# Kernel tuning notes

Measured on AMD Instinct MI355X. Metric: run time of the kernel, lower is better.

The kernel has to match this reference:

```python
import jax, jax.numpy as jnp
import numpy as np

SEQ_LEN, BATCH, INPUT, HID, LAYERS, TARGET_LEN = 120, 2048, 6, 64, 4, 120


def _cell(x_t, h, c, Wih, Whh, b):
    # torch LSTM gate order: input, forget, cell(g), output
    gates = x_t @ Wih.T + h @ Whh.T + b  # [B, 4H]
    i, f, g, o = jnp.split(gates, 4, axis=-1)
    c_new = jax.nn.sigmoid(f) * c + jax.nn.sigmoid(i) * jnp.tanh(g)
    h_new = jax.nn.sigmoid(o) * jnp.tanh(c_new)
    return h_new, c_new


def _stack_step(h, c, x_t, Wih0, Wih, Whh, b):
    # one time step through all stacked layers; h, c: [L, B, H]
    hs, cs = [], []
    inp = x_t
    L = Whh.shape[0]
    for l in range(L):
        W = Wih0 if l == 0 else Wih[l - 1]
        hn, cn = _cell(inp, h[l], c[l], W, Whh[l], b[l])
        hs.append(hn)
        cs.append(cn)
        inp = hn
    return jnp.stack(hs), jnp.stack(cs), inp


def setup_inputs() -> dict:
    key = jax.random.key(0)
    ks = jax.random.split(key, 11)
    s = 1.0 / np.sqrt(HID)  # torch LSTM uniform init scale
    u = lambda k, shp: jax.random.uniform(k, shp, jnp.float32, -s, s)
    return {
        "x": jax.random.normal(ks[0], (SEQ_LEN, BATCH, INPUT), jnp.float32),
        "enc_Wih0": u(ks[1], (4 * HID, INPUT)),
        "enc_Wih": u(ks[2], (LAYERS - 1, 4 * HID, HID)),
        "enc_Whh": u(ks[3], (LAYERS, 4 * HID, HID)),
        "enc_b": u(ks[4], (LAYERS, 4 * HID)),
        "dec_Wih0": u(ks[5], (4 * HID, INPUT)),
        "dec_Wih": u(ks[6], (LAYERS - 1, 4 * HID, HID)),
        "dec_Whh": u(ks[7], (LAYERS, 4 * HID, HID)),
        "dec_b": u(ks[8], (LAYERS, 4 * HID)),
        "lin_W": u(ks[9], (INPUT, HID)),
        "lin_b": u(ks[10], (INPUT,)),
        "target_len": TARGET_LEN,
    }


def reference(x, enc_Wih0, enc_Wih, enc_Whh, enc_b,
              dec_Wih0, dec_Wih, dec_Whh, dec_b, lin_W, lin_b, target_len):
    L, B, H = enc_Whh.shape[0], x.shape[1], enc_Whh.shape[-1]
    h0 = jnp.zeros((L, B, H), x.dtype)

    # ---- encoder: stacked LSTM over the input sequence (zero init state) ----
    def enc_step(carry, x_t):
        h, c = carry
        h, c, _ = _stack_step(h, c, x_t, enc_Wih0, enc_Wih, enc_Whh, enc_b)
        return (h, c), None

    (h, c), _ = jax.lax.scan(enc_step, (h0, h0), x)

    # ---- decoder: recursive one-step decode for target_len steps ----
    def dec_step(carry, _):
        h, c, inp = carry
        h, c, top = _stack_step(h, c, inp, dec_Wih0, dec_Wih, dec_Whh, dec_b)
        out = top @ lin_W.T + lin_b  # [B, INPUT]
        return (h, c, out), out

    last_in = x[-1]  # decoder seeded with last observed frame
    _, outputs = jax.lax.scan(dec_step, (h, c, last_in), None, length=target_len)
    return outputs  # [target_len, B, INPUT]
```

## Files before the change

### kernel.cpp

```cpp
#include <hip/hip_runtime.h>


#define S_LEN 120
#define BATCH 2048
#define NIN   6
#define H     64
#define NL    4
#define TLEN  120

#define HPAD 72

#define FRAGS_HALF 60
#define PACK_H8    (2 * FRAGS_HALF * 4 * 64)
#define PROJ_H8    (2 * 64)
#define NPACK      ((PACK_H8 + PROJ_H8) * 8)
#define EPACK_EL   (256 * 64 * 8)
#define NTOT       (NPACK + EPACK_EL)

#define PERM(kk) ((((kk) & 3) << 4) | ((kk) >> 2))
#define PI(c)    ((((c) & 15) << 2) | ((c) >> 4))

typedef _Float16 h8    __attribute__((ext_vector_type(8)));
typedef _Float16 h4    __attribute__((ext_vector_type(4)));
typedef float    f32x4 __attribute__((ext_vector_type(4)));

__global__ void prep_weights(const float* __restrict__ eWih0,
                             const float* __restrict__ eWih,
                             const float* __restrict__ eWhh,
                             const float* __restrict__ dWih0,
                             const float* __restrict__ dWih,
                             const float* __restrict__ dWhh,
                             const float* __restrict__ linW,
                             _Float16* __restrict__ wq) {
  int idx = blockIdx.x * blockDim.x + threadIdx.x;
  if (idx >= NTOT) return;

  if (idx >= NPACK) {
    int p    = idx - NPACK;
    int j    = p & 7;
    int lane = (p >> 3) & 63;
    int fe   = p >> 9;
    int kt   = fe & 3, nt = (fe >> 2) & 15, l = fe >> 6;
    int g    = nt * 16 + (lane & 15);
    int koff = ((lane >> 4) << 3) + j;
    float v = 0.0f;
    if (l == 0) {
      if (kt == 0)      v = (koff < NIN) ? eWih0[g * NIN + koff] : 0.0f;
      else if (kt == 1) v = 0.0f;
      else { int kk = (kt - 2) * 32 + koff; v = eWhh[g * H + PERM(kk)]; }
    } else {
      if (kt < 2) { int kk = kt * 32 + koff;
                    v = eWih[((l - 1) * 256 + g) * H + PERM(kk)]; }
      else        { int kk = (kt - 2) * 32 + koff;
                    v = eWhh[(l * 256 + g) * H + PERM(kk)]; }
    }
    wq[idx] = (_Float16)v;
    return;
  }

  if (idx >= PACK_H8 * 8) {
    int p    = idx - PACK_H8 * 8;
    int j    = p & 7;
    int lane = (p >> 3) & 63;
    int fr   = p >> 9;
    int m    = lane & 15;
    int k    = fr * 32 + ((lane >> 4) << 3) + j;
    wq[idx] = (_Float16)((m < NIN) ? linW[m * H + k] : 0.0f);
    return;
  }

  const int j    = idx & 7;
  const int lane = (idx >> 3) & 63;
  const int wv   = (idx >> 9) & 3;
  const int fh   = idx >> 11;
  const int f    = fh % FRAGS_HALF;
  const int half = fh / FRAGS_HALF;
  const float* Wi0 = half ? dWih0 : eWih0;
  const float* Wi  = half ? dWih  : eWih;
  const float* Wh  = half ? dWhh  : eWhh;
  int l, q, kt;
  if (f < 12) { l = 0; q = f / 3; kt = f % 3; }
  else        { int ff = f - 12; l = 1 + ff / 16; ff %= 16; q = ff / 4; kt = ff % 4; }
  const int g    = q * 64 + wv * 16 + (lane & 15);
  const int k_in = ((lane >> 4) << 3) + j;
  float v;
  if (l == 0) {
    if (kt == 0) v = (k_in < NIN) ? Wi0[g * NIN + k_in] : 0.0f;
    else         v = Wh[g * H + (kt - 1) * 32 + k_in];
  } else {
    if (kt < 2) v = Wi[((l - 1) * 256 + g) * H + kt * 32 + k_in];
    else        v = Wh[(l * 256 + g) * H + (kt - 2) * 32 + k_in];
  }
  wq[idx] = (_Float16)v;
}

__device__ __forceinline__ float rcpf(float x) { return __builtin_amdgcn_rcpf(x); }
__device__ __forceinline__ float sigf(float x) { return rcpf(1.0f + __expf(-x)); }
__device__ __forceinline__ float tanhf_(float x) {
  float e = __expf(2.0f * x);
  return 1.0f - 2.0f * rcpf(e + 1.0f);
}
__device__ __forceinline__ f32x4 mf(h8 a, h8 b, f32x4 c) {
  return __builtin_amdgcn_mfma_f32_16x16x32_f16(a, b, c, 0, 0, 0);
}
#define SPLAT(v) ((f32x4){(v), (v), (v), (v)})

__device__ __forceinline__ void cell_ew(f32x4 g0, f32x4 g1, f32x4 g2, f32x4 g3,
                                        f32x4& c, _Float16* outbuf,
                                        int quad, int r16, int wv) {
  #pragma unroll
  for (int r = 0; r < 4; r++) {
    float gi = sigf(g0[r]);
    float gf = sigf(g1[r]);
    float gg = tanhf_(g2[r]);
    float go = sigf(g3[r]);
    c[r] = fmaf(gf, c[r], gi * gg);
    outbuf[(quad * 4 + r) * HPAD + wv * 16 + r16] = (_Float16)(go * tanhf_(c[r]));
  }
}
__device__ __forceinline__ void fireH(const h8 (&w)[16], h8 ai0, h8 ai1,
                                      const f32x4 (&ac)[4], f32x4& c,
                                      _Float16* outbuf, int quad, int r16, int wv) {
  f32x4 g0 = mf(ai1, w[1],  mf(ai0, w[0],  ac[0]));
  f32x4 g1 = mf(ai1, w[5],  mf(ai0, w[4],  ac[1]));
  f32x4 g2 = mf(ai1, w[9],  mf(ai0, w[8],  ac[2]));
  f32x4 g3 = mf(ai1, w[13], mf(ai0, w[12], ac[3]));
  cell_ew(g0, g1, g2, g3, c, outbuf, quad, r16, wv);
}
__device__ __forceinline__ void precH(const h8 (&w)[16], h8 ar0, h8 ar1,
                                      f32x4 b, f32x4 (&ac)[4]) {
  ac[0] = mf(ar1, w[3],  mf(ar0, w[2],  SPLAT(b[0])));
  ac[1] = mf(ar1, w[7],  mf(ar0, w[6],  SPLAT(b[1])));
  ac[2] = mf(ar1, w[11], mf(ar0, w[10], SPLAT(b[2])));
  ac[3] = mf(ar1, w[15], mf(ar0, w[14], SPLAT(b[3])));
}
__device__ __forceinline__ void fire0(const h8 (&w)[12], h8 ax,
                                      const f32x4 (&ac)[4], f32x4& c,
                                      _Float16* outbuf, int quad, int r16, int wv) {
  f32x4 g0 = mf(ax, w[0], ac[0]);
  f32x4 g1 = mf(ax, w[3], ac[1]);
  f32x4 g2 = mf(ax, w[6], ac[2]);
  f32x4 g3 = mf(ax, w[9], ac[3]);
  cell_ew(g0, g1, g2, g3, c, outbuf, quad, r16, wv);
}
__device__ __forceinline__ void prec0(const h8 (&w)[12], h8 ar0, h8 ar1,
                                      f32x4 b, f32x4 (&ac)[4]) {
  ac[0] = mf(ar1, w[2],  mf(ar0, w[1],  SPLAT(b[0])));
  ac[1] = mf(ar1, w[5],  mf(ar0, w[4],  SPLAT(b[1])));
  ac[2] = mf(ar1, w[8],  mf(ar0, w[7],  SPLAT(b[2])));
  ac[3] = mf(ar1, w[11], mf(ar0, w[10], SPLAT(b[3])));
}
__device__ __forceinline__ void readA(const _Float16* buf, int r16, int quad,
                                      h8& a0, h8& a1) {
  a0 = *(const h8*)(buf + r16 * HPAD + quad * 8);
  a1 = *(const h8*)(buf + r16 * HPAD + 32 + quad * 8);
}

__global__ void __launch_bounds__(256, 1)
lstm_main(const float* __restrict__ X,
          const float* __restrict__ encb,
          const float* __restrict__ decb,
          const float* __restrict__ linb,
          const h8* __restrict__ WQ,
          float* __restrict__ out) {
  __shared__ _Float16 Hb[NL][2][16][HPAD];
  __shared__ _Float16 Xb[2][16][HPAD];
  __shared__ float    Cx[NL][16][68];

  const int tid   = threadIdx.x;
  const int wv    = tid >> 6;
  const int lane  = tid & 63;
  const int quad  = lane >> 4;
  const int r16   = lane & 15;
  const int bbase = blockIdx.x * 16;

  {
    float* p = (float*)&Hb[0][0][0][0];
    for (int i = tid; i < (int)(NL * 2 * 16 * HPAD / 2); i += 256) p[i] = 0.0f;
    float* px = (float*)&Xb[0][0][0];
    for (int i = tid; i < (int)(2 * 16 * HPAD / 2); i += 256) px[i] = 0.0f;
  }
  if (tid < 96) {
    const int m = tid / NIN, i = tid - m * NIN;
    Xb[0][m][i] = (_Float16)X[((size_t)0 * BATCH + bbase + m) * NIN + i];
  }

  h8 we[16][4];
  #pragma unroll
  for (int nt = 0; nt < 16; nt++)
    #pragma unroll
    for (int kt = 0; kt < 4; kt++)
      we[nt][kt] = WQ[(PACK_H8 + PROJ_H8) + ((wv * 64 + nt * 4 + kt) * 64 + lane)];

  float ben[16];
  #pragma unroll
  for (int nt = 0; nt < 16; nt++) ben[nt] = encb[wv * 256 + nt * 16 + r16];

  f32x4 ce[4];
  #pragma unroll
  for (int ct = 0; ct < 4; ct++) ce[ct] = SPLAT(0.f);

  __syncthreads();

  #pragma unroll 1
  for (int i = 0; i < S_LEN + NL - 1; i++) {
    const int p = i & 1;
    const bool active = (i >= wv) && (i - wv < S_LEN);
    if (active) {
      const _Float16* inb = (wv == 0) ? &Xb[p][0][0] : &Hb[wv - 1][p ^ 1][0][0];
      const _Float16* rcb = &Hb[wv][p ^ 1][0][0];
      h8 ai0 = *(const h8*)(inb + r16 * HPAD + quad * 8);
      h8 ai1 = *(const h8*)(inb + r16 * HPAD + 32 + quad * 8);
      h8 ar0 = *(const h8*)(rcb + r16 * HPAD + quad * 8);
      h8 ar1 = *(const h8*)(rcb + r16 * HPAD + 32 + quad * 8);

      float pf0 = 0.f, pf1 = 0.f;
      const bool doPf = (wv == 0) && (lane < 48) && (i + 1 < S_LEN);
      if (doPf) {
        const float* xs = X + ((size_t)(i + 1) * BATCH + bbase) * NIN;
        pf0 = xs[lane * 2];
        pf1 = xs[lane * 2 + 1];
      }

      f32x4 acc[16];
      #pragma unroll
      for (int nt = 0; nt < 16; nt++) {
        f32x4 a = SPLAT(ben[nt]);
        a = mf(ai0, we[nt][0], a);
        a = mf(ai1, we[nt][1], a);
        a = mf(ar0, we[nt][2], a);
        a = mf(ar1, we[nt][3], a);
        acc[nt] = a;
      }

      _Float16* wb = &Hb[wv][p][0][0];
      #pragma unroll
      for (int r = 0; r < 4; r++) {
        h4 hv;
        #pragma unroll
        for (int ct = 0; ct < 4; ct++) {
          float gi = sigf(acc[ct][r]);
          float gf = sigf(acc[4 + ct][r]);
          float gg = tanhf_(acc[8 + ct][r]);
          float go = sigf(acc[12 + ct][r]);
          ce[ct][r] = fmaf(gf, ce[ct][r], gi * gg);
          hv[ct] = (_Float16)(go * tanhf_(ce[ct][r]));
        }
        *(h4*)(wb + (quad * 4 + r) * HPAD + 4 * r16) = hv;
      }

      if (doPf) {
        int e0 = lane * 2, e1 = e0 + 1;
        Xb[p ^ 1][e0 / NIN][e0 % NIN] = (_Float16)pf0;
        Xb[p ^ 1][e1 / NIN][e1 % NIN] = (_Float16)pf1;
      }
    }
    __syncthreads();
  }

  #pragma unroll
  for (int ct = 0; ct < 4; ct++)
    #pragma unroll
    for (int r = 0; r < 4; r++)
      Cx[wv][quad * 4 + r][ct * 16 + r16] = ce[ct][r];

  float hreg[16];
  #pragma unroll
  for (int u = 0; u < 16; u++) {
    int i2 = tid + u * 256;
    int l = i2 >> 10, m = (i2 >> 6) & 15, c = i2 & 63;
    hreg[u] = (float)Hb[l][(l + 1) & 1][m][PI(c)];
  }
  __syncthreads();
  #pragma unroll
  for (int u = 0; u < 16; u++) {
    int i2 = tid + u * 256;
    int l = i2 >> 10, m = (i2 >> 6) & 15, c = i2 & 63;
    Hb[l][1][m][c] = (_Float16)hreg[u];
  }
  __syncthreads();

  f32x4 cs0, cs1, cs2, cs3;
  #pragma unroll
  for (int r = 0; r < 4; r++) {
    cs0[r] = Cx[0][quad * 4 + r][wv * 16 + r16];
    cs1[r] = Cx[1][quad * 4 + r][wv * 16 + r16];
    cs2[r] = Cx[2][quad * 4 + r][wv * 16 + r16];
    cs3[r] = Cx[3][quad * 4 + r][wv * 16 + r16];
  }

  h8 w0[12], w1[16], w2[16], w3[16];
  #pragma unroll
  for (int f = 0; f < 12; f++) w0[f] = WQ[((FRAGS_HALF + f)      * 4 + wv) * 64 + lane];
  #pragma unroll
  for (int f = 0; f < 16; f++) w1[f] = WQ[((FRAGS_HALF + 12 + f) * 4 + wv) * 64 + lane];
  #pragma unroll
  for (int f = 0; f < 16; f++) w2[f] = WQ[((FRAGS_HALF + 28 + f) * 4 + wv) * 64 + lane];
  #pragma unroll
  for (int f = 0; f < 16; f++) w3[f] = WQ[((FRAGS_HALF + 44 + f) * 4 + wv) * 64 + lane];

  f32x4 b0, b1, b2, b3;
  #pragma unroll
  for (int q = 0; q < 4; q++) {
    b0[q] = decb[0 * 256 + q * 64 + wv * 16 + r16];
    b1[q] = decb[1 * 256 + q * 64 + wv * 16 + r16];
    b2[q] = decb[2 * 256 + q * 64 + wv * 16 + r16];
    b3[q] = decb[3 * 256 + q * 64 + wv * 16 + r16];
  }

  h8 lwA0 = WQ[PACK_H8 + lane];
  h8 lwA1 = WQ[PACK_H8 + 64 + lane];
  f32x4 lbq;
  #pragma unroll
  for (int r = 0; r < 4; r++)
    lbq[r] = (quad * 4 + r < NIN) ? linb[quad * 4 + r] : 0.0f;

  f32x4 ac0[4], ac1[4], ac2[4], ac3[4];
  {
    h8 s0, s1;
    readA(&Hb[0][1][0][0], r16, quad, s0, s1); prec0(w0, s0, s1, b0, ac0);
    readA(&Hb[1][1][0][0], r16, quad, s0, s1); precH(w1, s0, s1, b1, ac1);
    readA(&Hb[2][1][0][0], r16, quad, s0, s1); precH(w2, s0, s1, b2, ac2);
  }
  __syncthreads();

  #pragma unroll 1
  for (int t = 0; t < TLEN; t++) {
    const int cur = t & 1, prv = cur ^ 1;
    {
      h8 ar0, ar1;
      readA(&Hb[3][prv][0][0], r16, quad, ar0, ar1);
      h8 ax;
      if (t == 0) {
        ax = *(const h8*)(&Xb[1][0][0] + r16 * HPAD + quad * 8);
      } else {
        f32x4 ap = lbq;
        ap = mf(lwA0, ar0, ap);
        ap = mf(lwA1, ar1, ap);
        if (wv == 0) {
          #pragma unroll
          for (int r = 0; r < 4; r++) {
            const int fm = quad * 4 + r;
            if (fm < NIN)
              out[((size_t)(t - 1) * BATCH + bbase + r16) * NIN + fm] = ap[r];
          }
        }
        float x0 = __shfl(ap[0], r16);
        float x1 = __shfl(ap[1], r16);
        float x2 = __shfl(ap[2], r16);
        float x3 = __shfl(ap[3], r16);
        float x4 = __shfl(ap[0], 16 + r16);
        float x5 = __shfl(ap[1], 16 + r16);
        h8 xa = {};
        xa[0] = (_Float16)x0; xa[1] = (_Float16)x1; xa[2] = (_Float16)x2;
        xa[3] = (_Float16)x3; xa[4] = (_Float16)x4; xa[5] = (_Float16)x5;
        h8 zz = {};
        ax = (quad == 0) ? xa : zz;
      }
      precH(w3, ar0, ar1, b3, ac3);
      fire0(w0, ax, ac0, cs0, &Hb[0][cur][0][0], quad, r16, wv);
      __syncthreads();
    }
    {
      h8 ai0, ai1;
      readA(&Hb[0][cur][0][0], r16, quad, ai0, ai1);
      fireH(w1, ai0, ai1, ac1, cs1, &Hb[1][cur][0][0], quad, r16, wv);
      prec0(w0, ai0, ai1, b0, ac0);
      __syncthreads();
    }
    {
      h8 ai0, ai1;
      readA(&Hb[1][cur][0][0], r16, quad, ai0, ai1);
      fireH(w2, ai0, ai1, ac2, cs2, &Hb[2][cur][0][0], quad, r16, wv);
      precH(w1, ai0, ai1, b1, ac1);
      __syncthreads();
    }
    {
      h8 ai0, ai1;
      readA(&Hb[2][cur][0][0], r16, quad, ai0, ai1);
      fireH(w3, ai0, ai1, ac3, cs3, &Hb[3][cur][0][0], quad, r16, wv);
      precH(w2, ai0, ai1, b2, ac2);
      __syncthreads();
    }
  }

  if (wv == 0) {
    h8 ar0, ar1;
    readA(&Hb[3][1][0][0], r16, quad, ar0, ar1);
    f32x4 ap = lbq;
    ap = mf(lwA0, ar0, ap);
    ap = mf(lwA1, ar1, ap);
    #pragma unroll
    for (int r = 0; r < 4; r++) {
      const int fm = quad * 4 + r;
      if (fm < NIN)
        out[((size_t)(TLEN - 1) * BATCH + bbase + r16) * NIN + fm] = ap[r];
    }
  }
}

extern "C" void kernel_launch(void* const* d_in, const int* in_sizes, int n_in,
                              void* d_out, int out_size, void* d_ws, size_t ws_size,
                              hipStream_t stream) {
  const float* X     = (const float*)d_in[0];
  const float* eWih0 = (const float*)d_in[1];
  const float* eWih  = (const float*)d_in[2];
  const float* eWhh  = (const float*)d_in[3];
  const float* eb    = (const float*)d_in[4];
  const float* dWih0 = (const float*)d_in[5];
  const float* dWih  = (const float*)d_in[6];
  const float* dWhh  = (const float*)d_in[7];
  const float* db    = (const float*)d_in[8];
  const float* lW    = (const float*)d_in[9];
  const float* lb    = (const float*)d_in[10];

  _Float16* wq = (_Float16*)d_ws;

  prep_weights<<<(NTOT + 255) / 256, 256, 0, stream>>>(
      eWih0, eWih, eWhh, dWih0, dWih, dWhh, lW, wq);

  lstm_main<<<BATCH / 16, 256, 0, stream>>>(
      X, eb, db, lb, (const h8*)wq, (float*)d_out);
}
```

Before: 579.4 us.

## Fuse gate activations, prefetch X two steps ahead, use lighter LDS-only barriers

Replaces __syncthreads with an inline s_waitcnt lgkmcnt(0) plus s_barrier, so barriers no longer wait on outstanding global memory operations. Moves the X prefetch one step further ahead so its global load latency overlaps a full iteration. Rewrites the LSTM elementwise math to combine the sigmoid and tanh reciprocals, using fewer rcp instructions per cell, with clamping added to avoid overflow. Risks: the hand-written barrier relies on global stores not needing ordering before the barrier, and the clamp slightly changes numerics.

Result: slower. 593.4 us (+2.4%).

```diff
diff --git a/kernel.cpp b/kernel.cpp
--- a/kernel.cpp
+++ b/kernel.cpp
@@ -23,6 +23,10 @@
 typedef _Float16 h8    __attribute__((ext_vector_type(8)));
 typedef _Float16 h4    __attribute__((ext_vector_type(4)));
 typedef float    f32x4 __attribute__((ext_vector_type(4)));
+
+__device__ __forceinline__ void bar_lgkm() {
+  asm volatile("s_waitcnt lgkmcnt(0)\n\ts_barrier" ::: "memory");
+}
 
 __global__ void prep_weights(const float* __restrict__ eWih0,
                              const float* __restrict__ eWih,
@@ -95,27 +99,33 @@
 }
 
 __device__ __forceinline__ float rcpf(float x) { return __builtin_amdgcn_rcpf(x); }
-__device__ __forceinline__ float sigf(float x) { return rcpf(1.0f + __expf(-x)); }
-__device__ __forceinline__ float tanhf_(float x) {
-  float e = __expf(2.0f * x);
-  return 1.0f - 2.0f * rcpf(e + 1.0f);
-}
 __device__ __forceinline__ f32x4 mf(h8 a, h8 b, f32x4 c) {
   return __builtin_amdgcn_mfma_f32_16x16x32_f16(a, b, c, 0, 0, 0);
 }
 #define SPLAT(v) ((f32x4){(v), (v), (v), (v)})
+
+__device__ __forceinline__ float ew_one(float gi, float gf, float gg, float go,
+                                        float& c) {
+  gg = fminf(fmaxf(gg, -20.0f), 20.0f);
+  float eni = __expf(-gi);
+  float e2g = __expf(2.0f * gg);
+  float enf = __expf(-gf);
+  float eno = __expf(-go);
+  c = c * rcpf(1.0f + enf) + (e2g - 1.0f) * rcpf((1.0f + eni) * (e2g + 1.0f));
+  float cc = fminf(fmaxf(c, -20.0f), 20.0f);
+  float e2c = __expf(2.0f * cc);
+  return (e2c - 1.0f) * rcpf((1.0f + eno) * (e2c + 1.0f));
+}
 
 __device__ __forceinline__ void cell_ew(f32x4 g0, f32x4 g1, f32x4 g2, f32x4 g3,
                                         f32x4& c, _Float16* outbuf,
                                         int quad, int r16, int wv) {
   #pragma unroll
   for (int r = 0; r < 4; r++) {
-    float gi = sigf(g0[r]);
-    float gf = sigf(g1[r]);
-    float gg = tanhf_(g2[r]);
-    float go = sigf(g3[r]);
-    c[r] = fmaf(gf, c[r], gi * gg);
-    outbuf[(quad * 4 + r) * HPAD + wv * 16 + r16] = (_Float16)(go * tanhf_(c[r]));
+    float cv = c[r];
+    float hv = ew_one(g0[r], g1[r], g2[r], g3[r], cv);
+    c[r] = cv;
+    outbuf[(quad * 4 + r) * HPAD + wv * 16 + r16] = (_Float16)hv;
   }
 }
 __device__ __forceinline__ void fireH(const h8 (&w)[16], h8 ai0, h8 ai1,
@@ -199,6 +209,16 @@
   f32x4 ce[4];
   #pragma unroll
   for (int ct = 0; ct < 4; ct++) ce[ct] = SPLAT(0.f);
+
+  const bool pfLane = (wv == 0) && (lane < 48);
+  const int pe0 = lane * 2, pe1 = pe0 + 1;
+  const int pm0 = pe0 / NIN, pc0 = pe0 % NIN;
+  const int pm1 = pe1 / NIN, pc1 = pe1 % NIN;
+  float pf0 = 0.f, pf1 = 0.f;
+  if (pfLane) {
+    const float* xs = X + ((size_t)1 * BATCH + bbase) * NIN;
+    pf0 = xs[pe0]; pf1 = xs[pe1];
+  }
 
   __syncthreads();
 
@@ -214,12 +234,10 @@
       h8 ar0 = *(const h8*)(rcb + r16 * HPAD + quad * 8);
       h8 ar1 = *(const h8*)(rcb + r16 * HPAD + 32 + quad * 8);
 
-      float pf0 = 0.f, pf1 = 0.f;
-      const bool doPf = (wv == 0) && (lane < 48) && (i + 1 < S_LEN);
-      if (doPf) {
-        const float* xs = X + ((size_t)(i + 1) * BATCH + bbase) * NIN;
-        pf0 = xs[lane * 2];
-        pf1 = xs[lane * 2 + 1];
+      float nf0 = 0.f, nf1 = 0.f;
+      if (pfLane && (i + 2 < S_LEN)) {
+        const float* xs = X + ((size_t)(i + 2) * BATCH + bbase) * NIN;
+        nf0 = xs[pe0]; nf1 = xs[pe1];
       }
 
       f32x4 acc[16];
@@ -239,23 +257,21 @@
         h4 hv;
         #pragma unroll
         for (int ct = 0; ct < 4; ct++) {
-          float gi = sigf(acc[ct][r]);
-          float gf = sigf(acc[4 + ct][r]);
-          float gg = tanhf_(acc[8 + ct][r]);
-          float go = sigf(acc[12 + ct][r]);
-          ce[ct][r] = fmaf(gf, ce[ct][r], gi * gg);
-          hv[ct] = (_Float16)(go * tanhf_(ce[ct][r]));
+          float cv = ce[ct][r];
+          hv[ct] = (_Float16)ew_one(acc[ct][r], acc[4 + ct][r],
+                                    acc[8 + ct][r], acc[12 + ct][r], cv);
+          ce[ct][r] = cv;
         }
         *(h4*)(wb + (quad * 4 + r) * HPAD + 4 * r16) = hv;
       }
 
-      if (doPf) {
-        int e0 = lane * 2, e1 = e0 + 1;
-        Xb[p ^ 1][e0 / NIN][e0 % NIN] = (_Float16)pf0;
-        Xb[p ^ 1][e1 / NIN][e1 % NIN] = (_Float16)pf1;
+      if (pfLane && (i + 1 < S_LEN)) {
+        Xb[p ^ 1][pm0][pc0] = (_Float16)pf0;
+        Xb[p ^ 1][pm1][pc1] = (_Float16)pf1;
       }
-    }
-    __syncthreads();
+      pf0 = nf0; pf1 = nf1;
+    }
+    bar_lgkm();
   }
 
   #pragma unroll
@@ -359,28 +375,28 @@
       }
       precH(w3, ar0, ar1, b3, ac3);
       fire0(w0, ax, ac0, cs0, &Hb[0][cur][0][0], quad, r16, wv);
-      __syncthreads();
+      bar_lgkm();
     }
     {
       h8 ai0, ai1;
       readA(&Hb[0][cur][0][0], r16, quad, ai0, ai1);
       fireH(w1, ai0, ai1, ac1, cs1, &Hb[1][cur][0][0], quad, r16, wv);
       prec0(w0, ai0, ai1, b0, ac0);
-      __syncthreads();
+      bar_lgkm();
     }
     {
       h8 ai0, ai1;
       readA(&Hb[1][cur][0][0], r16, quad, ai0, ai1);
       fireH(w2, ai0, ai1, ac2, cs2, &Hb[2][cur][0][0], quad, r16, wv);
       precH(w1, ai0, ai1, b1, ac1);
-      __syncthreads();
+      bar_lgkm();
     }
     {
       h8 ai0, ai1;
       readA(&Hb[2][cur][0][0], r16, quad, ai0, ai1);
       fireH(w3, ai0, ai1, ac3, cs3, &Hb[3][cur][0][0], quad, r16, wv);
       precH(w2, ai0, ai1, b2, ac2);
-      __syncthreads();
+      bar_lgkm();
     }
   }
 
```
